# Optimization experiments

Hardware: AMD Instinct MI355X
Metric: run time of the kernel (lower is better)

The kernel has to match this reference:

```python
import jax, jax.numpy as jnp
import numpy as np

N = 50000      # nodes
E = 800000     # edges
F = 128        # node feature dim (= output_size, residual)
H = 128        # hidden_size

def _uniform_fan_avg(key, shape):
    # VarianceScaling(scale=1.0, mode='fan_avg', distribution='uniform')
    fan_avg = (shape[0] + shape[1]) / 2.0
    limit = np.sqrt(3.0 / fan_avg)
    return jax.random.uniform(key, shape, jnp.float32, -limit, limit)

def setup_inputs() -> dict:
    key = jax.random.key(0)
    ks = jax.random.split(key, 16)
    h = jax.random.normal(ks[0], (N, F), jnp.float32)
    pos = jax.random.normal(ks[1], (N, 3), jnp.float32)
    senders = jax.random.randint(ks[2], (E,), 0, N, jnp.int32)
    receivers = jax.random.randint(ks[3], (E,), 0, N, jnp.int32)
    # edge_mlp: Linear(2F+1 -> H) silu, Linear(H -> H) silu (activate_final=True)
    eW1 = _uniform_fan_avg(ks[4], (2 * F + 1, H)); eb1 = jnp.zeros((H,), jnp.float32)
    eW2 = _uniform_fan_avg(ks[5], (H, H)); eb2 = jnp.zeros((H,), jnp.float32)
    # node_mlp: Linear(F+H -> H) silu, Linear(H -> F) (no final act)
    nW1 = _uniform_fan_avg(ks[6], (F + H, H)); nb1 = jnp.zeros((H,), jnp.float32)
    nW2 = _uniform_fan_avg(ks[7], (H, F)); nb2 = jnp.zeros((F,), jnp.float32)
    # pos_correction_mlp: Linear(H -> H) silu, Linear(H -> 1, no bias, UniformScaling(dt))
    pW1 = _uniform_fan_avg(ks[8], (H, H)); pb1 = jnp.zeros((H,), jnp.float32)
    dt = 0.001
    pW2 = jax.random.uniform(ks[9], (H, 1), jnp.float32, -dt, dt) * np.sqrt(3.0)
    return {"h": h, "pos": pos, "senders": senders, "receivers": receivers,
            "eW1": eW1, "eb1": eb1, "eW2": eW2, "eb2": eb2,
            "nW1": nW1, "nb1": nb1, "nW2": nW2, "nb2": nb2,
            "pW1": pW1, "pb1": pb1, "pW2": pW2}

def reference(h, pos, senders, receivers,
              eW1, eb1, eW2, eb2,
              nW1, nb1, nW2, nb2,
              pW1, pb1, pW2):
    n = h.shape[0]
    # _coord2radial (normalize=False)
    coord_diff = pos[senders] - pos[receivers]            # [E,3]
    radial = jnp.sum(coord_diff ** 2, axis=1, keepdims=True)  # [E,1]
    # edge update (_message): concat(h[senders], h[receivers], radial) -> edge_mlp
    msg_in = jnp.concatenate([h[senders], h[receivers], radial], axis=-1)  # [E,2F+1]
    msg = jax.nn.silu(msg_in @ eW1 + eb1)
    msg = jax.nn.silu(msg @ eW2 + eb2)                    # [E,H]
    # node update (_update): aggregate messages at receivers, node_mlp, residual
    agg = jax.ops.segment_sum(msg, receivers, num_segments=n)  # [N,H]
    x = jnp.concatenate([h, agg], axis=-1)                # [N,F+H]
    x = jax.nn.silu(x @ nW1 + nb1)
    x = x @ nW2 + nb2                                     # [N,F]
    h_new = h + x                                         # residual
    # position update (_pos_update)
    pc = jax.nn.silu(msg @ pW1 + pb1) @ pW2               # [E,1]
    trans = jnp.clip(coord_diff * pc, -100, 100)          # [E,3]
    pos_new = pos + jax.ops.segment_sum(trans, senders, num_segments=n)
    return h_new, pos_new
```

## Files before the change

### kernel.cpp

```cpp
#include <hip/hip_runtime.h>
#include <hip/hip_bf16.h>

#define NNODES 50000
#define NEDGES 800000
#define EB 1024
#define SCAN_BLOCKS 196
#define TRN_BLOCKS 448

typedef short bf16x8 __attribute__((ext_vector_type(8)));
typedef float f32x4 __attribute__((ext_vector_type(4)));
typedef unsigned short u16;
typedef unsigned int u32;

__device__ __forceinline__ u16 f2bf(float f) {
    __hip_bfloat16 b = __float2bfloat16(f);
    return *reinterpret_cast<u16*>(&b);
}
__device__ __forceinline__ float bf2f(u16 v) {
    u32 u = ((u32)v) << 16;
    return __uint_as_float(u);
}
__device__ __forceinline__ u32 pack2(float a, float b) {
    __hip_bfloat162 t = __float22bfloat162_rn(float2{a, b});
    return *reinterpret_cast<u32*>(&t);
}
__device__ __forceinline__ float fast_silu(float x) {
    float e = __builtin_amdgcn_exp2f(-1.442695040888963f * x);
    return x * __builtin_amdgcn_rcpf(1.0f + e);
}
__device__ __forceinline__ bf16x8 ld8(const u16* p) {
    return *(const bf16x8*)p;
}
__device__ __forceinline__ f32x4 mfma16(bf16x8 a, bf16x8 b, f32x4 c) {
    return __builtin_amdgcn_mfma_f32_16x16x32_bf16(a, b, c, 0, 0, 0);
}

__global__ void prep_kernel(const float* __restrict__ eW1, const float* __restrict__ eW2,
                            const float* __restrict__ pW1, const float* __restrict__ nW1,
                            const float* __restrict__ nW2,
                            u16* __restrict__ eW1T, u16* __restrict__ eW2T,
                            u16* __restrict__ pW1T, u16* __restrict__ nW1T,
                            u16* __restrict__ nW2T,
                            const int* __restrict__ rcv, int* __restrict__ counts) {
    int b = blockIdx.x;
    if (b < TRN_BLOCKS) {
        int i = b * 256 + threadIdx.x;
        const float* src; u16* dst; int K;
        if (i < 32768)      { src = eW1; dst = eW1T; K = 256; }
        else if (i < 49152) { src = eW2; dst = eW2T; K = 128; i -= 32768; }
        else if (i < 65536) { src = pW1; dst = pW1T; K = 128; i -= 49152; }
        else if (i < 98304) { src = nW1; dst = nW1T; K = 256; i -= 65536; }
        else                { src = nW2; dst = nW2T; K = 128; i -= 98304; }
        int n = i / K, k = i - n * K;
        dst[i] = f2bf(src[k * 128 + n]);
    } else {
        int e = (b - TRN_BLOCKS) * 256 + threadIdx.x;
        if (e < NEDGES) atomicAdd(&counts[rcv[e]], 1);
    }
}

__global__ __launch_bounds__(256) void gemm_p(
    const float* __restrict__ h, const u16* __restrict__ eW1T,
    const u16* __restrict__ nW1T, const float* __restrict__ eb1,
    u16* __restrict__ P)
{
    const int tid  = threadIdx.x;
    const int w    = tid >> 6;
    const int lane = tid & 63;
    const int m    = lane & 15;
    const int quad = lane >> 4;
    const int ksub = quad * 8;

    bf16x8 bw[4][6];
    float bias[6];
    #pragma unroll
    for (int cc = 0; cc < 6; cc++) {
        int C = 96 * w + 16 * cc + m;
        const u16* bp;
        if (C < 128)      { bp = eW1T + C * 256;               bias[cc] = 0.5f * eb1[C]; }
        else if (C < 256) { bp = eW1T + (C - 128) * 256 + 128; bias[cc] = 0.5f * eb1[C - 128]; }
        else              { bp = nW1T + (C - 256) * 256;       bias[cc] = 0.f; }
        #pragma unroll
        for (int t = 0; t < 4; t++) bw[t][cc] = ld8(bp + t * 32 + ksub);
    }
    const int base = blockIdx.x * 64;
    #pragma unroll
    for (int mt = 0; mt < 4; mt++) {
        int nm = base + mt * 16 + m;
        if (nm >= NNODES) nm = NNODES - 1;
        bf16x8 afr[4];
        #pragma unroll
        for (int t = 0; t < 4; t++) {
            const float* ap = h + (size_t)nm * 128 + t * 32 + ksub;
            f32x4 lo = *(const f32x4*)ap;
            f32x4 hi = *(const f32x4*)(ap + 4);
            #pragma unroll
            for (int j = 0; j < 4; j++) {
                afr[t][j]     = (short)f2bf(lo[j]);
                afr[t][4 + j] = (short)f2bf(hi[j]);
            }
        }
        f32x4 acc[6];
        #pragma unroll
        for (int cc = 0; cc < 6; cc++) acc[cc] = (f32x4){0,0,0,0};
        #pragma unroll
        for (int t = 0; t < 4; t++)
            #pragma unroll
            for (int cc = 0; cc < 6; cc++)
                acc[cc] = mfma16(afr[t], bw[t][cc], acc[cc]);
        #pragma unroll
        for (int cc = 0; cc < 6; cc++) {
            int C = 96 * w + 16 * cc + m;
            #pragma unroll
            for (int r = 0; r < 4; r++) {
                int nr = base + mt * 16 + quad * 4 + r;
                if (nr < NNODES) P[(size_t)nr * 384 + C] = f2bf(acc[cc][r] + bias[cc]);
            }
        }
    }
}

__global__ void scan1(const int* __restrict__ counts, int* __restrict__ excl,
                      int* __restrict__ blkSum) {
    __shared__ int tmp[256];
    int tx = threadIdx.x;
    int i = blockIdx.x * 256 + tx;
    int v = (i < NNODES) ? counts[i] : 0;
    tmp[tx] = v;
    __syncthreads();
    for (int off = 1; off < 256; off <<= 1) {
        int t = (tx >= off) ? tmp[tx - off] : 0;
        __syncthreads();
        tmp[tx] += t;
        __syncthreads();
    }
    if (i < NNODES) excl[i] = tmp[tx] - v;
    if (tx == 255) blkSum[blockIdx.x] = tmp[255];
}
__global__ void scan2(const int* __restrict__ blkSum, int* __restrict__ blkOff) {
    __shared__ int tmp[256];
    int tx = threadIdx.x;
    int v = (tx < SCAN_BLOCKS) ? blkSum[tx] : 0;
    tmp[tx] = v;
    __syncthreads();
    for (int off = 1; off < 256; off <<= 1) {
        int t = (tx >= off) ? tmp[tx - off] : 0;
        __syncthreads();
        tmp[tx] += t;
        __syncthreads();
    }
    if (tx < SCAN_BLOCKS) blkOff[tx] = tmp[tx] - v;
}
__global__ void scan3(const int* __restrict__ excl, const int* __restrict__ blkOff,
                      int* __restrict__ cursor) {
    int i = blockIdx.x * 256 + threadIdx.x;
    if (i < NNODES) cursor[i] = excl[i] + blkOff[blockIdx.x];
}
__global__ void scatter_kernel(const int* __restrict__ rcv, int* __restrict__ cursor,
                               int* __restrict__ perm) {
    int e = blockIdx.x * 256 + threadIdx.x;
    if (e < NEDGES) {
        int p = atomicAdd(&cursor[rcv[e]], 1);
        perm[p] = e;
    }
}

struct __align__(16) EdgeLds {
    u16   m1[64 * 136];
    u16   msg[64 * 136];
    float diff[64][4];
    float pcpart[4][64];
    float wlast[128];
    float radial[64];
    int   sndloc[64];
    int   rcvloc[64];
};

__global__ __launch_bounds__(256, 4) void edge_kernel(
    const u16* __restrict__ P, const float* __restrict__ pos,
    const int* __restrict__ snd, const int* __restrict__ rcv,
    const int* __restrict__ perm,
    const float* __restrict__ eW1last,
    const u16* __restrict__ eW2T, const float* __restrict__ eb2,
    const u16* __restrict__ pW1T, const float* __restrict__ pb1,
    const float* __restrict__ pW2,
    float* __restrict__ agg, float* __restrict__ posacc)
{
    __shared__ EdgeLds S;
    const int tid  = threadIdx.x;
    const int w    = tid >> 6;
    const int lane = tid & 63;
    const int m    = lane & 15;
    const int quad = lane >> 4;
    const int ksub = quad * 8;

    bf16x8 bw2[4][2], bp1[4][2];
    float b2v[2], pb1v[2], pw2v[2];
    #pragma unroll
    for (int cc = 0; cc < 2; cc++) {
        int col = (2 * w + cc) * 16 + m;
        #pragma unroll
        for (int t = 0; t < 4; t++) {
            bw2[t][cc] = ld8(eW2T + col * 128 + t * 32 + ksub);
            bp1[t][cc] = ld8(pW1T + col * 128 + t * 32 + ksub);
        }
        b2v[cc]  = eb2[col];
        pb1v[cc] = pb1[col];
        pw2v[cc] = pW2[col];
    }
    if (tid < 128) S.wlast[tid] = eW1last[tid];

    for (int base = blockIdx.x * 64; base < NEDGES; base += gridDim.x * 64) {
        __syncthreads();
        const int e = lane;
        int eg = perm[base + e];
        int s = snd[eg], r = rcv[eg];
        if (tid < 64) {
            S.sndloc[tid] = s; S.rcvloc[tid] = r;
            float rad = 0.f;
            #pragma unroll
            for (int c = 0; c < 3; c++) {
                float d = pos[s * 3 + c] - pos[r * 3 + c];
                S.diff[tid][c] = d;
                rad += d * d;
            }
            S.radial[tid] = rad;
        }
        __syncthreads();
        {
            float rad = S.radial[e];
            const u16* pa = P + (size_t)s * 384 + w * 32;
            const u16* pb = P + (size_t)r * 384 + 128 + w * 32;
            const int sw = e >> 3;
            #pragma unroll
            for (int k = 0; k < 4; k++) {
                bf16x8 va = ld8(pa + k * 8);
                bf16x8 vb = ld8(pb + k * 8);
                u32 pk[4];
                #pragma unroll
                for (int jj = 0; jj < 4; jj++) {
                    int col = w * 32 + k * 8 + jj * 2;
                    float2 wl = *(const float2*)&S.wlast[col];
                    float v0 = bf2f((u16)va[jj * 2])     + bf2f((u16)vb[jj * 2])     + rad * wl.x;
                    float v1 = bf2f((u16)va[jj * 2 + 1]) + bf2f((u16)vb[jj * 2 + 1]) + rad * wl.y;
                    pk[jj] = pack2(fast_silu(v0), fast_silu(v1));
                }
                int chunk = (w * 4 + k) ^ sw;
                *(uint4*)&S.m1[e * 136 + chunk * 8] =
                    make_uint4(pk[0], pk[1], pk[2], pk[3]);
            }
        }
        __syncthreads();
        #pragma unroll
        for (int mt = 0; mt < 4; mt++) {
            const int rs = mt * 2 + (m >> 3);
            const int row = mt * 16 + m;
            f32x4 acc0 = (f32x4){0,0,0,0}, acc1 = (f32x4){0,0,0,0};
            #pragma unroll
            for (int t = 0; t < 4; t++) {
                bf16x8 a = *(const bf16x8*)&S.m1[row * 136 + ((t * 4 + quad) ^ rs) * 8];
                acc0 = mfma16(a, bw2[t][0], acc0);
                acc1 = mfma16(a, bw2[t][1], acc1);
            }
            #pragma unroll
            for (int cc = 0; cc < 2; cc++) {
                f32x4 acc = cc ? acc1 : acc0;
                int col = (2 * w + cc) * 16 + m;
                #pragma unroll
                for (int rr = 0; rr < 4; rr++) {
                    int orow = mt * 16 + quad * 4 + rr;
                    S.msg[orow * 136 + col] = f2bf(fast_silu(acc[rr] + b2v[cc]));
                }
            }
        }
        __syncthreads();
        #pragma unroll
        for (int mt = 0; mt < 4; mt++) {
            f32x4 acc0 = (f32x4){0,0,0,0}, acc1 = (f32x4){0,0,0,0};
            #pragma unroll
            for (int t = 0; t < 4; t++) {
                bf16x8 a = *(const bf16x8*)&S.msg[(mt * 16 + m) * 136 + t * 32 + ksub];
                acc0 = mfma16(a, bp1[t][0], acc0);
                acc1 = mfma16(a, bp1[t][1], acc1);
            }
            float p4[4];
            #pragma unroll
            for (int rr = 0; rr < 4; rr++)
                p4[rr] = fast_silu(acc0[rr] + pb1v[0]) * pw2v[0]
                       + fast_silu(acc1[rr] + pb1v[1]) * pw2v[1];
            #pragma unroll
            for (int mask = 1; mask < 16; mask <<= 1) {
                #pragma unroll
                for (int rr = 0; rr < 4; rr++) p4[rr] += __shfl_xor(p4[rr], mask);
            }
            if (m == 0) {
                #pragma unroll
                for (int rr = 0; rr < 4; rr++)
                    S.pcpart[w][mt * 16 + quad * 4 + rr] = p4[rr];
            }
        }
        {
            int half = tid >> 7, col = tid & 127;
            int r0 = half * 32;
            float a = 0.f;
            int cur = S.rcvloc[r0];
            for (int rr = r0; rr < r0 + 32; ++rr) {
                int rc = S.rcvloc[rr];
                if (rc != cur) {
                    atomicAdd(&agg[(size_t)cur * 128 + col], a);
                    a = 0.f; cur = rc;
                }
                a += bf2f(S.msg[rr * 136 + col]);
            }
            atomicAdd(&agg[(size_t)cur * 128 + col], a);
        }
        __syncthreads();
        if (tid < 192) {
            int ee = tid / 3, c = tid - ee * 3;
            float pc = S.pcpart[0][ee] + S.pcpart[1][ee] + S.pcpart[2][ee] + S.pcpart[3][ee];
            float tr = S.diff[ee][c] * pc;
            tr = fminf(fmaxf(tr, -100.f), 100.f);
            atomicAdd(&posacc[S.sndloc[ee] * 3 + c], tr);
        }
    }
}

__global__ __launch_bounds__(256, 4) void node_kernel(
    const u16* __restrict__ P, const float* __restrict__ h,
    const float* __restrict__ agg,
    const u16* __restrict__ nW1T, const float* __restrict__ nb1,
    const u16* __restrict__ nW2T, const float* __restrict__ nb2,
    const float* __restrict__ pos, const float* __restrict__ posacc,
    float* __restrict__ out)
{
    __shared__ alignas(16) u16 m1[64 * 136];
    const int tid  = threadIdx.x;
    const int w    = tid >> 6;
    const int lane = tid & 63;
    const int m    = lane & 15;
    const int quad = lane >> 4;
    const int ksub = quad * 8;

    bf16x8 bw1[4][2], bw2[4][2];
    float b1v[2], b2v[2];
    #pragma unroll
    for (int cc = 0; cc < 2; cc++) {
        int col = (2 * w + cc) * 16 + m;
        #pragma unroll
        for (int t = 0; t < 4; t++) {
            bw1[t][cc] = ld8(nW1T + col * 256 + 128 + t * 32 + ksub);
            bw2[t][cc] = ld8(nW2T + col * 128 + t * 32 + ksub);
        }
        b1v[cc] = nb1[col];
        b2v[cc] = nb2[col];
    }
    const int base = blockIdx.x * 64;
    #pragma unroll
    for (int mt = 0; mt < 4; mt++) {
        int nm = base + mt * 16 + m;
        if (nm >= NNODES) nm = NNODES - 1;
        f32x4 acc0 = (f32x4){0,0,0,0}, acc1 = (f32x4){0,0,0,0};
        #pragma unroll
        for (int t = 0; t < 4; t++) {
            const float* ap = agg + (size_t)nm * 128 + t * 32 + ksub;
            f32x4 lo = *(const f32x4*)ap;
            f32x4 hi = *(const f32x4*)(ap + 4);
            bf16x8 a;
            #pragma unroll
            for (int j = 0; j < 4; j++) {
                a[j]     = (short)f2bf(lo[j]);
                a[4 + j] = (short)f2bf(hi[j]);
            }
            acc0 = mfma16(a, bw1[t][0], acc0);
            acc1 = mfma16(a, bw1[t][1], acc1);
        }
        #pragma unroll
        for (int cc = 0; cc < 2; cc++) {
            f32x4 acc = cc ? acc1 : acc0;
            int col = (2 * w + cc) * 16 + m;
            #pragma unroll
            for (int rr = 0; rr < 4; rr++) {
                int row = mt * 16 + quad * 4 + rr;
                int nrc = base + row; if (nrc >= NNODES) nrc = NNODES - 1;
                float v = acc[rr] + bf2f(P[(size_t)nrc * 384 + 256 + col]) + b1v[cc];
                m1[row * 136 + col] = f2bf(fast_silu(v));
            }
        }
    }
    __syncthreads();
    #pragma unroll
    for (int mt = 0; mt < 4; mt++) {
        f32x4 acc0 = (f32x4){0,0,0,0}, acc1 = (f32x4){0,0,0,0};
        #pragma unroll
        for (int t = 0; t < 4; t++) {
            bf16x8 a = *(const bf16x8*)&m1[(mt * 16 + m) * 136 + t * 32 + ksub];
            acc0 = mfma16(a, bw2[t][0], acc0);
            acc1 = mfma16(a, bw2[t][1], acc1);
        }
        #pragma unroll
        for (int cc = 0; cc < 2; cc++) {
            f32x4 acc = cc ? acc1 : acc0;
            int col = (2 * w + cc) * 16 + m;
            #pragma unroll
            for (int rr = 0; rr < 4; rr++) {
                int nr = base + mt * 16 + quad * 4 + rr;
                if (nr < NNODES)
                    out[(size_t)nr * 128 + col] = acc[rr] + b2v[cc] + h[(size_t)nr * 128 + col];
            }
        }
    }
    if (tid < 192) {
        int i = blockIdx.x * 192 + tid;
        if (i < NNODES * 3) out[NNODES * 128 + i] = pos[i] + posacc[i];
    }
}

extern "C" void kernel_launch(void* const* d_in, const int* in_sizes, int n_in,
                              void* d_out, int out_size, void* d_ws, size_t ws_size,
                              hipStream_t stream) {
    (void)in_sizes; (void)n_in; (void)out_size; (void)ws_size;
    const float* h   = (const float*)d_in[0];
    const float* pos = (const float*)d_in[1];
    const int*   snd = (const int*)d_in[2];
    const int*   rcv = (const int*)d_in[3];
    const float* eW1 = (const float*)d_in[4];
    const float* eb1 = (const float*)d_in[5];
    const float* eW2 = (const float*)d_in[6];
    const float* eb2 = (const float*)d_in[7];
    const float* nW1 = (const float*)d_in[8];
    const float* nb1 = (const float*)d_in[9];
    const float* nW2 = (const float*)d_in[10];
    const float* nb2 = (const float*)d_in[11];
    const float* pW1 = (const float*)d_in[12];
    const float* pb1 = (const float*)d_in[13];
    const float* pW2 = (const float*)d_in[14];
    float* out = (float*)d_out;

    float* agg    = (float*)d_ws;
    float* posacc = agg + (size_t)NNODES * 128;
    u16* P    = (u16*)(posacc + (size_t)NNODES * 3);
    u16* eW1T = P + (size_t)NNODES * 384;
    u16* eW2T = eW1T + 128 * 256;
    u16* pW1T = eW2T + 128 * 128;
    u16* nW1T = pW1T + 128 * 128;
    u16* nW2T = nW1T + 128 * 256;
    int* counts = (int*)(nW2T + 128 * 128);
    int* excl   = counts + 50048;
    int* blkSum = excl + 50048;
    int* blkOff = blkSum + 256;
    int* cursor = blkOff + 256;
    int* perm   = cursor + 50048;

    hipMemsetAsync(agg, 0, (size_t)NNODES * 131 * sizeof(float), stream);
    hipMemsetAsync(counts, 0, 50048 * sizeof(int), stream);

    prep_kernel<<<TRN_BLOCKS + (NEDGES + 255) / 256, 256, 0, stream>>>(
        eW1, eW2, pW1, nW1, nW2, eW1T, eW2T, pW1T, nW1T, nW2T, rcv, counts);

    gemm_p<<<(NNODES + 63) / 64, 256, 0, stream>>>(h, eW1T, nW1T, eb1, P);

    scan1<<<SCAN_BLOCKS, 256, 0, stream>>>(counts, excl, blkSum);
    scan2<<<1, 256, 0, stream>>>(blkSum, blkOff);
    scan3<<<SCAN_BLOCKS, 256, 0, stream>>>(excl, blkOff, cursor);
    scatter_kernel<<<(NEDGES + 255) / 256, 256, 0, stream>>>(rcv, cursor, perm);

    edge_kernel<<<EB, 256, 0, stream>>>(
        P, pos, snd, rcv, perm,
        eW1 + 256 * 128,
        eW2T, eb2, pW1T, pb1, pW2,
        agg, posacc);

    node_kernel<<<(NNODES + 63) / 64, 256, 0, stream>>>(
        P, h, agg, nW1T, nb1, nW2T, nb2, pos, posacc, out);
}
```

Measured before the change: 449.8 us.

## Fuse all stages into one cooperative persistent kernel with grid-wide phases

Replaces the chain of separate launches and memsets (weight transpose, count, gemm, three scan kernels, scatter, edge, node) with a single persistent kernel that runs each stage as a phase, separated by grid syncs when cooperative launch is available. It also zeroes the accumulators in-kernel, overlaps edge counting with the node GEMM, and merges scan3 into the scatter by adding block offsets inline. The goal is to remove per-launch overhead and idle gaps between small kernels. In exchange, grid syncs add cost, the grid is limited to what fits resident (which may lower occupancy), and the GEMM phase reloads weights per tile in halves.

```diff
diff --git a/kernel.cpp b/kernel.cpp
--- a/kernel.cpp
+++ b/kernel.cpp
@@ -1,11 +1,14 @@
 #include <hip/hip_runtime.h>
 #include <hip/hip_bf16.h>
+#include <hip/hip_cooperative_groups.h>
+
+namespace cg = cooperative_groups;
 
 #define NNODES 50000
 #define NEDGES 800000
-#define EB 1024
-#define SCAN_BLOCKS 196
-#define TRN_BLOCKS 448
+#define NTILE_N 782
+#define TRN_ITEMS 114688
+#define ZWORDS4 1650012
 
 typedef short bf16x8 __attribute__((ext_vector_type(8)));
 typedef float f32x4 __attribute__((ext_vector_type(4)));
@@ -35,135 +38,15 @@
     return __builtin_amdgcn_mfma_f32_16x16x32_bf16(a, b, c, 0, 0, 0);
 }
 
-__global__ void prep_kernel(const float* __restrict__ eW1, const float* __restrict__ eW2,
-                            const float* __restrict__ pW1, const float* __restrict__ nW1,
-                            const float* __restrict__ nW2,
-                            u16* __restrict__ eW1T, u16* __restrict__ eW2T,
-                            u16* __restrict__ pW1T, u16* __restrict__ nW1T,
-                            u16* __restrict__ nW2T,
-                            const int* __restrict__ rcv, int* __restrict__ counts) {
-    int b = blockIdx.x;
-    if (b < TRN_BLOCKS) {
-        int i = b * 256 + threadIdx.x;
-        const float* src; u16* dst; int K;
-        if (i < 32768)      { src = eW1; dst = eW1T; K = 256; }
-        else if (i < 49152) { src = eW2; dst = eW2T; K = 128; i -= 32768; }
-        else if (i < 65536) { src = pW1; dst = pW1T; K = 128; i -= 49152; }
-        else if (i < 98304) { src = nW1; dst = nW1T; K = 256; i -= 65536; }
-        else                { src = nW2; dst = nW2T; K = 128; i -= 98304; }
-        int n = i / K, k = i - n * K;
-        dst[i] = f2bf(src[k * 128 + n]);
-    } else {
-        int e = (b - TRN_BLOCKS) * 256 + threadIdx.x;
-        if (e < NEDGES) atomicAdd(&counts[rcv[e]], 1);
-    }
-}
-
-__global__ __launch_bounds__(256) void gemm_p(
-    const float* __restrict__ h, const u16* __restrict__ eW1T,
-    const u16* __restrict__ nW1T, const float* __restrict__ eb1,
-    u16* __restrict__ P)
-{
-    const int tid  = threadIdx.x;
-    const int w    = tid >> 6;
-    const int lane = tid & 63;
-    const int m    = lane & 15;
-    const int quad = lane >> 4;
-    const int ksub = quad * 8;
-
-    bf16x8 bw[4][6];
-    float bias[6];
-    #pragma unroll
-    for (int cc = 0; cc < 6; cc++) {
-        int C = 96 * w + 16 * cc + m;
-        const u16* bp;
-        if (C < 128)      { bp = eW1T + C * 256;               bias[cc] = 0.5f * eb1[C]; }
-        else if (C < 256) { bp = eW1T + (C - 128) * 256 + 128; bias[cc] = 0.5f * eb1[C - 128]; }
-        else              { bp = nW1T + (C - 256) * 256;       bias[cc] = 0.f; }
-        #pragma unroll
-        for (int t = 0; t < 4; t++) bw[t][cc] = ld8(bp + t * 32 + ksub);
-    }
-    const int base = blockIdx.x * 64;
-    #pragma unroll
-    for (int mt = 0; mt < 4; mt++) {
-        int nm = base + mt * 16 + m;
-        if (nm >= NNODES) nm = NNODES - 1;
-        bf16x8 afr[4];
-        #pragma unroll
-        for (int t = 0; t < 4; t++) {
-            const float* ap = h + (size_t)nm * 128 + t * 32 + ksub;
-            f32x4 lo = *(const f32x4*)ap;
-            f32x4 hi = *(const f32x4*)(ap + 4);
-            #pragma unroll
-            for (int j = 0; j < 4; j++) {
-                afr[t][j]     = (short)f2bf(lo[j]);
-                afr[t][4 + j] = (short)f2bf(hi[j]);
-            }
-        }
-        f32x4 acc[6];
-        #pragma unroll
-        for (int cc = 0; cc < 6; cc++) acc[cc] = (f32x4){0,0,0,0};
-        #pragma unroll
-        for (int t = 0; t < 4; t++)
-            #pragma unroll
-            for (int cc = 0; cc < 6; cc++)
-                acc[cc] = mfma16(afr[t], bw[t][cc], acc[cc]);
-        #pragma unroll
-        for (int cc = 0; cc < 6; cc++) {
-            int C = 96 * w + 16 * cc + m;
-            #pragma unroll
-            for (int r = 0; r < 4; r++) {
-                int nr = base + mt * 16 + quad * 4 + r;
-                if (nr < NNODES) P[(size_t)nr * 384 + C] = f2bf(acc[cc][r] + bias[cc]);
-            }
-        }
-    }
-}
-
-__global__ void scan1(const int* __restrict__ counts, int* __restrict__ excl,
-                      int* __restrict__ blkSum) {
-    __shared__ int tmp[256];
-    int tx = threadIdx.x;
-    int i = blockIdx.x * 256 + tx;
-    int v = (i < NNODES) ? counts[i] : 0;
-    tmp[tx] = v;
-    __syncthreads();
-    for (int off = 1; off < 256; off <<= 1) {
-        int t = (tx >= off) ? tmp[tx - off] : 0;
-        __syncthreads();
-        tmp[tx] += t;
-        __syncthreads();
-    }
-    if (i < NNODES) excl[i] = tmp[tx] - v;
-    if (tx == 255) blkSum[blockIdx.x] = tmp[255];
-}
-__global__ void scan2(const int* __restrict__ blkSum, int* __restrict__ blkOff) {
-    __shared__ int tmp[256];
-    int tx = threadIdx.x;
-    int v = (tx < SCAN_BLOCKS) ? blkSum[tx] : 0;
-    tmp[tx] = v;
-    __syncthreads();
-    for (int off = 1; off < 256; off <<= 1) {
-        int t = (tx >= off) ? tmp[tx - off] : 0;
-        __syncthreads();
-        tmp[tx] += t;
-        __syncthreads();
-    }
-    if (tx < SCAN_BLOCKS) blkOff[tx] = tmp[tx] - v;
-}
-__global__ void scan3(const int* __restrict__ excl, const int* __restrict__ blkOff,
-                      int* __restrict__ cursor) {
-    int i = blockIdx.x * 256 + threadIdx.x;
-    if (i < NNODES) cursor[i] = excl[i] + blkOff[blockIdx.x];
-}
-__global__ void scatter_kernel(const int* __restrict__ rcv, int* __restrict__ cursor,
-                               int* __restrict__ perm) {
-    int e = blockIdx.x * 256 + threadIdx.x;
-    if (e < NEDGES) {
-        int p = atomicAdd(&cursor[rcv[e]], 1);
-        perm[p] = e;
-    }
-}
+struct MegaParams {
+    const float *h, *pos;
+    const int *snd, *rcv;
+    const float *eW1, *eb1, *eW2, *eb2, *nW1, *nb1, *nW2, *nb2, *pW1, *pb1, *pW2;
+    float *agg, *posacc;
+    int *counts, *excl, *blkSum, *blkOff, *perm;
+    u16 *P, *eW1T, *eW2T, *pW1T, *nW1T, *nW2T;
+    float *out;
+};
 
 struct __align__(16) EdgeLds {
     u16   m1[64 * 136];
@@ -176,242 +59,338 @@
     int   rcvloc[64];
 };
 
-__global__ __launch_bounds__(256, 4) void edge_kernel(
-    const u16* __restrict__ P, const float* __restrict__ pos,
-    const int* __restrict__ snd, const int* __restrict__ rcv,
-    const int* __restrict__ perm,
-    const float* __restrict__ eW1last,
-    const u16* __restrict__ eW2T, const float* __restrict__ eb2,
-    const u16* __restrict__ pW1T, const float* __restrict__ pb1,
-    const float* __restrict__ pW2,
-    float* __restrict__ agg, float* __restrict__ posacc)
-{
-    __shared__ EdgeLds S;
+union SharedU {
+    EdgeLds edge;
+    int     scan[256];
+    u16     nm1[64 * 136];
+};
+
+__global__ __launch_bounds__(256, 4) void mega(MegaParams p, int plo, int phi) {
+    __shared__ SharedU U;
     const int tid  = threadIdx.x;
+    const int gid  = blockIdx.x * 256 + tid;
+    const int gsz  = gridDim.x * 256;
     const int w    = tid >> 6;
     const int lane = tid & 63;
     const int m    = lane & 15;
     const int quad = lane >> 4;
     const int ksub = quad * 8;
 
-    bf16x8 bw2[4][2], bp1[4][2];
-    float b2v[2], pb1v[2], pw2v[2];
-    #pragma unroll
-    for (int cc = 0; cc < 2; cc++) {
-        int col = (2 * w + cc) * 16 + m;
-        #pragma unroll
-        for (int t = 0; t < 4; t++) {
-            bw2[t][cc] = ld8(eW2T + col * 128 + t * 32 + ksub);
-            bp1[t][cc] = ld8(pW1T + col * 128 + t * 32 + ksub);
-        }
-        b2v[cc]  = eb2[col];
-        pb1v[cc] = pb1[col];
-        pw2v[cc] = pW2[col];
-    }
-    if (tid < 128) S.wlast[tid] = eW1last[tid];
-
-    for (int base = blockIdx.x * 64; base < NEDGES; base += gridDim.x * 64) {
-        __syncthreads();
-        const int e = lane;
-        int eg = perm[base + e];
-        int s = snd[eg], r = rcv[eg];
-        if (tid < 64) {
-            S.sndloc[tid] = s; S.rcvloc[tid] = r;
-            float rad = 0.f;
-            #pragma unroll
-            for (int c = 0; c < 3; c++) {
-                float d = pos[s * 3 + c] - pos[r * 3 + c];
-                S.diff[tid][c] = d;
-                rad += d * d;
-            }
-            S.radial[tid] = rad;
-        }
-        __syncthreads();
-        {
-            float rad = S.radial[e];
-            const u16* pa = P + (size_t)s * 384 + w * 32;
-            const u16* pb = P + (size_t)r * 384 + 128 + w * 32;
-            const int sw = e >> 3;
-            #pragma unroll
-            for (int k = 0; k < 4; k++) {
-                bf16x8 va = ld8(pa + k * 8);
-                bf16x8 vb = ld8(pb + k * 8);
-                u32 pk[4];
-                #pragma unroll
-                for (int jj = 0; jj < 4; jj++) {
-                    int col = w * 32 + k * 8 + jj * 2;
-                    float2 wl = *(const float2*)&S.wlast[col];
-                    float v0 = bf2f((u16)va[jj * 2])     + bf2f((u16)vb[jj * 2])     + rad * wl.x;
-                    float v1 = bf2f((u16)va[jj * 2 + 1]) + bf2f((u16)vb[jj * 2 + 1]) + rad * wl.y;
-                    pk[jj] = pack2(fast_silu(v0), fast_silu(v1));
-                }
-                int chunk = (w * 4 + k) ^ sw;
-                *(uint4*)&S.m1[e * 136 + chunk * 8] =
-                    make_uint4(pk[0], pk[1], pk[2], pk[3]);
-            }
-        }
-        __syncthreads();
-        #pragma unroll
-        for (int mt = 0; mt < 4; mt++) {
-            const int rs = mt * 2 + (m >> 3);
-            const int row = mt * 16 + m;
-            f32x4 acc0 = (f32x4){0,0,0,0}, acc1 = (f32x4){0,0,0,0};
-            #pragma unroll
-            for (int t = 0; t < 4; t++) {
-                bf16x8 a = *(const bf16x8*)&S.m1[row * 136 + ((t * 4 + quad) ^ rs) * 8];
-                acc0 = mfma16(a, bw2[t][0], acc0);
-                acc1 = mfma16(a, bw2[t][1], acc1);
-            }
+    for (int ph = plo; ph <= phi; ph++) {
+        if (ph == 1) {
+            f32x4* z = (f32x4*)p.agg;
+            for (int i = gid; i < ZWORDS4; i += gsz) z[i] = (f32x4){0,0,0,0};
+            for (int i = gid; i < TRN_ITEMS; i += gsz) {
+                int j = i, n, k;
+                const float* src; u16* dst;
+                if (i < 32768)       { src = p.eW1; dst = p.eW1T; n = j >> 8; k = j & 255; }
+                else if (i < 49152)  { j -= 32768; src = p.eW2; dst = p.eW2T; n = j >> 7; k = j & 127; }
+                else if (i < 65536)  { j -= 49152; src = p.pW1; dst = p.pW1T; n = j >> 7; k = j & 127; }
+                else if (i < 98304)  { j -= 65536; src = p.nW1; dst = p.nW1T; n = j >> 8; k = j & 255; }
+                else                 { j -= 98304; src = p.nW2; dst = p.nW2T; n = j >> 7; k = j & 127; }
+                dst[j] = f2bf(src[k * 128 + n]);
+            }
+        } else if (ph == 2) {
+            for (int e = gid; e < NEDGES; e += gsz)
+                atomicAdd(&p.counts[p.rcv[e]], 1);
+            for (int it = blockIdx.x; it < NTILE_N; it += gridDim.x) {
+                const int base = it * 64;
+                #pragma unroll
+                for (int half = 0; half < 2; half++) {
+                    bf16x8 bw[4][3];
+                    float bias[3];
+                    #pragma unroll
+                    for (int cc = 0; cc < 3; cc++) {
+                        int C = 96 * w + 48 * half + 16 * cc + m;
+                        const u16* bp;
+                        if (C < 128)      { bp = p.eW1T + C * 256;               bias[cc] = 0.5f * p.eb1[C]; }
+                        else if (C < 256) { bp = p.eW1T + (C - 128) * 256 + 128; bias[cc] = 0.5f * p.eb1[C - 128]; }
+                        else              { bp = p.nW1T + (C - 256) * 256;       bias[cc] = 0.f; }
+                        #pragma unroll
+                        for (int t = 0; t < 4; t++) bw[t][cc] = ld8(bp + t * 32 + ksub);
+                    }
+                    #pragma unroll
+                    for (int mt = 0; mt < 4; mt++) {
+                        int nm = base + mt * 16 + m;
+                        if (nm >= NNODES) nm = NNODES - 1;
+                        bf16x8 afr[4];
+                        #pragma unroll
+                        for (int t = 0; t < 4; t++) {
+                            const float* ap = p.h + (size_t)nm * 128 + t * 32 + ksub;
+                            f32x4 lo = *(const f32x4*)ap;
+                            f32x4 hi = *(const f32x4*)(ap + 4);
+                            #pragma unroll
+                            for (int j = 0; j < 4; j++) {
+                                afr[t][j]     = (short)f2bf(lo[j]);
+                                afr[t][4 + j] = (short)f2bf(hi[j]);
+                            }
+                        }
+                        f32x4 acc[3];
+                        #pragma unroll
+                        for (int cc = 0; cc < 3; cc++) acc[cc] = (f32x4){0,0,0,0};
+                        #pragma unroll
+                        for (int t = 0; t < 4; t++)
+                            #pragma unroll
+                            for (int cc = 0; cc < 3; cc++)
+                                acc[cc] = mfma16(afr[t], bw[t][cc], acc[cc]);
+                        #pragma unroll
+                        for (int cc = 0; cc < 3; cc++) {
+                            int C = 96 * w + 48 * half + 16 * cc + m;
+                            #pragma unroll
+                            for (int r = 0; r < 4; r++) {
+                                int nr = base + mt * 16 + quad * 4 + r;
+                                if (nr < NNODES) p.P[(size_t)nr * 384 + C] = f2bf(acc[cc][r] + bias[cc]);
+                            }
+                        }
+                    }
+                }
+            }
+        } else if (ph == 3) {
+            for (int b = blockIdx.x; b < 196; b += gridDim.x) {
+                __syncthreads();
+                int i = b * 256 + tid;
+                int v = (i < NNODES) ? p.counts[i] : 0;
+                U.scan[tid] = v;
+                __syncthreads();
+                for (int off = 1; off < 256; off <<= 1) {
+                    int t = (tid >= off) ? U.scan[tid - off] : 0;
+                    __syncthreads();
+                    U.scan[tid] += t;
+                    __syncthreads();
+                }
+                if (i < NNODES) p.excl[i] = U.scan[tid] - v;
+                if (tid == 255) p.blkSum[b] = U.scan[255];
+            }
+        } else if (ph == 4) {
+            if (blockIdx.x == 0) {
+                int v = (tid < 196) ? p.blkSum[tid] : 0;
+                U.scan[tid] = v;
+                __syncthreads();
+                for (int off = 1; off < 256; off <<= 1) {
+                    int t = (tid >= off) ? U.scan[tid - off] : 0;
+                    __syncthreads();
+                    U.scan[tid] += t;
+                    __syncthreads();
+                }
+                if (tid < 196) p.blkOff[tid] = U.scan[tid] - v;
+            }
+        } else if (ph == 5) {
+            for (int e = gid; e < NEDGES; e += gsz) {
+                int r = p.rcv[e];
+                int pi = atomicAdd(&p.excl[r], 1) + p.blkOff[r >> 8];
+                p.perm[pi] = e;
+            }
+        } else if (ph == 6) {
+            EdgeLds& S = U.edge;
+            const float* eW1last = p.eW1 + 256 * 128;
+            bf16x8 bw2[4][2], bp1[4][2];
+            float b2v[2], pb1v[2], pw2v[2];
             #pragma unroll
             for (int cc = 0; cc < 2; cc++) {
-                f32x4 acc = cc ? acc1 : acc0;
                 int col = (2 * w + cc) * 16 + m;
                 #pragma unroll
-                for (int rr = 0; rr < 4; rr++) {
-                    int orow = mt * 16 + quad * 4 + rr;
-                    S.msg[orow * 136 + col] = f2bf(fast_silu(acc[rr] + b2v[cc]));
-                }
-            }
+                for (int t = 0; t < 4; t++) {
+                    bw2[t][cc] = ld8(p.eW2T + col * 128 + t * 32 + ksub);
+                    bp1[t][cc] = ld8(p.pW1T + col * 128 + t * 32 + ksub);
+                }
+                b2v[cc]  = p.eb2[col];
+                pb1v[cc] = p.pb1[col];
+                pw2v[cc] = p.pW2[col];
+            }
+            if (tid < 128) S.wlast[tid] = eW1last[tid];
+
+            for (int base = blockIdx.x * 64; base < NEDGES; base += gridDim.x * 64) {
+                __syncthreads();
+                const int e = lane;
+                int eg = p.perm[base + e];
+                int s = p.snd[eg], r = p.rcv[eg];
+                if (tid < 64) {
+                    S.sndloc[tid] = s; S.rcvloc[tid] = r;
+                    float rad = 0.f;
+                    #pragma unroll
+                    for (int c = 0; c < 3; c++) {
+                        float d = p.pos[s * 3 + c] - p.pos[r * 3 + c];
+                        S.diff[tid][c] = d;
+                        rad += d * d;
+                    }
+                    S.radial[tid] = rad;
+                }
+                __syncthreads();
+                {
+                    float rad = S.radial[e];
+                    const u16* pa = p.P + (size_t)s * 384 + w * 32;
+                    const u16* pb = p.P + (size_t)r * 384 + 128 + w * 32;
+                    const int sw = e >> 3;
+                    #pragma unroll
+                    for (int k = 0; k < 4; k++) {
+                        bf16x8 va = ld8(pa + k * 8);
+                        bf16x8 vb = ld8(pb + k * 8);
+                        u32 pk[4];
+                        #pragma unroll
+                        for (int jj = 0; jj < 4; jj++) {
+                            int col = w * 32 + k * 8 + jj * 2;
+                            float2 wl = *(const float2*)&S.wlast[col];
+                            float v0 = bf2f((u16)va[jj * 2])     + bf2f((u16)vb[jj * 2])     + rad * wl.x;
+                            float v1 = bf2f((u16)va[jj * 2 + 1]) + bf2f((u16)vb[jj * 2 + 1]) + rad * wl.y;
+                            pk[jj] = pack2(fast_silu(v0), fast_silu(v1));
+                        }
+                        int chunk = (w * 4 + k) ^ sw;
+                        *(uint4*)&S.m1[e * 136 + chunk * 8] =
+                            make_uint4(pk[0], pk[1], pk[2], pk[3]);
+                    }
+                }
+                __syncthreads();
+                #pragma unroll
+                for (int mt = 0; mt < 4; mt++) {
+                    const int rs = mt * 2 + (m >> 3);
+                    const int row = mt * 16 + m;
+                    f32x4 acc0 = (f32x4){0,0,0,0}, acc1 = (f32x4){0,0,0,0};
+                    #pragma unroll
+                    for (int t = 0; t < 4; t++) {
+                        bf16x8 a = *(const bf16x8*)&S.m1[row * 136 + ((t * 4 + quad) ^ rs) * 8];
+                        acc0 = mfma16(a, bw2[t][0], acc0);
+                        acc1 = mfma16(a, bw2[t][1], acc1);
+                    }
+                    #pragma unroll
+                    for (int cc = 0; cc < 2; cc++) {
+                        f32x4 acc = cc ? acc1 : acc0;
+                        int col = (2 * w + cc) * 16 + m;
+                        #pragma unroll
+                        for (int rr = 0; rr < 4; rr++) {
+                            int orow = mt * 16 + quad * 4 + rr;
+                            S.msg[orow * 136 + col] = f2bf(fast_silu(acc[rr] + b2v[cc]));
+                        }
+                    }
+                }
+                __syncthreads();
+                #pragma unroll
+                for (int mt = 0; mt < 4; mt++) {
+                    f32x4 acc0 = (f32x4){0,0,0,0}, acc1 = (f32x4){0,0,0,0};
+                    #pragma unroll
+                    for (int t = 0; t < 4; t++) {
+                        bf16x8 a = *(const bf16x8*)&S.msg[(mt * 16 + m) * 136 + t * 32 + ksub];
+                        acc0 = mfma16(a, bp1[t][0], acc0);
+                        acc1 = mfma16(a, bp1[t][1], acc1);
+                    }
+                    float p4[4];
+                    #pragma unroll
+                    for (int rr = 0; rr < 4; rr++)
+                        p4[rr] = fast_silu(acc0[rr] + pb1v[0]) * pw2v[0]
+                               + fast_silu(acc1[rr] + pb1v[1]) * pw2v[1];
+                    #pragma unroll
+                    for (int mask = 1; mask < 16; mask <<= 1) {
+                        #pragma unroll
+                        for (int rr = 0; rr < 4; rr++) p4[rr] += __shfl_xor(p4[rr], mask);
+                    }
+                    if (m == 0) {
+                        #pragma unroll
+                        for (int rr = 0; rr < 4; rr++)
+                            S.pcpart[w][mt * 16 + quad * 4 + rr] = p4[rr];
+                    }
+                }
+                {
+                    int half = tid >> 7, col = tid & 127;
+                    int r0 = half * 32;
+                    float a = 0.f;
+                    int cur = S.rcvloc[r0];
+                    for (int rr = r0; rr < r0 + 32; ++rr) {
+                        int rc = S.rcvloc[rr];
+                        if (rc != cur) {
+                            atomicAdd(&p.agg[(size_t)cur * 128 + col], a);
+                            a = 0.f; cur = rc;
+                        }
+                        a += bf2f(S.msg[rr * 136 + col]);
+                    }
+                    atomicAdd(&p.agg[(size_t)cur * 128 + col], a);
+                }
+                __syncthreads();
+                if (tid < 192) {
+                    int ee = tid / 3, c = tid - ee * 3;
+                    float pc = S.pcpart[0][ee] + S.pcpart[1][ee] + S.pcpart[2][ee] + S.pcpart[3][ee];
+                    float tr = S.diff[ee][c] * pc;
+                    tr = fminf(fmaxf(tr, -100.f), 100.f);
+                    atomicAdd(&p.posacc[S.sndloc[ee] * 3 + c], tr);
+                }
+            }
+        } else if (ph == 7) {
+            bf16x8 bw1[4][2], bw2[4][2];
+            float b1v[2], b2v[2];
+            #pragma unroll
+            for (int cc = 0; cc < 2; cc++) {
+                int col = (2 * w + cc) * 16 + m;
+                #pragma unroll
+                for (int t = 0; t < 4; t++) {
+                    bw1[t][cc] = ld8(p.nW1T + col * 256 + 128 + t * 32 + ksub);
+                    bw2[t][cc] = ld8(p.nW2T + col * 128 + t * 32 + ksub);
+                }
+                b1v[cc] = p.nb1[col];
+                b2v[cc] = p.nb2[col];
+            }
+            for (int it = blockIdx.x; it < NTILE_N; it += gridDim.x) {
+                const int base = it * 64;
+                __syncthreads();
+                #pragma unroll
+                for (int mt = 0; mt < 4; mt++) {
+                    int nm = base + mt * 16 + m;
+                    if (nm >= NNODES) nm = NNODES - 1;
+                    f32x4 acc0 = (f32x4){0,0,0,0}, acc1 = (f32x4){0,0,0,0};
+                    #pragma unroll
+                    for (int t = 0; t < 4; t++) {
+                        const float* ap = p.agg + (size_t)nm * 128 + t * 32 + ksub;
+                        f32x4 lo = *(const f32x4*)ap;
+                        f32x4 hi = *(const f32x4*)(ap + 4);
+                        bf16x8 a;
+                        #pragma unroll
+                        for (int j = 0; j < 4; j++) {
+                            a[j]     = (short)f2bf(lo[j]);
+                            a[4 + j] = (short)f2bf(hi[j]);
+                        }
+                        acc0 = mfma16(a, bw1[t][0], acc0);
+                        acc1 = mfma16(a, bw1[t][1], acc1);
+                    }
+                    #pragma unroll
+                    for (int cc = 0; cc < 2; cc++) {
+                        f32x4 acc = cc ? acc1 : acc0;
+                        int col = (2 * w + cc) * 16 + m;
+                        #pragma unroll
+                        for (int rr = 0; rr < 4; rr++) {
+                            int row = mt * 16 + quad * 4 + rr;
+                            int nrc = base + row; if (nrc >= NNODES) nrc = NNODES - 1;
+                            float v = acc[rr] + bf2f(p.P[(size_t)nrc * 384 + 256 + col]) + b1v[cc];
+                            U.nm1[row * 136 + col] = f2bf(fast_silu(v));
+                        }
+                    }
+                }
+                __syncthreads();
+                #pragma unroll
+                for (int mt = 0; mt < 4; mt++) {
+                    f32x4 acc0 = (f32x4){0,0,0,0}, acc1 = (f32x4){0,0,0,0};
+                    #pragma unroll
+                    for (int t = 0; t < 4; t++) {
+                        bf16x8 a = *(const bf16x8*)&U.nm1[(mt * 16 + m) * 136 + t * 32 + ksub];
+                        acc0 = mfma16(a, bw2[t][0], acc0);
+                        acc1 = mfma16(a, bw2[t][1], acc1);
+                    }
+                    #pragma unroll
+                    for (int cc = 0; cc < 2; cc++) {
+                        f32x4 acc = cc ? acc1 : acc0;
+                        int col = (2 * w + cc) * 16 + m;
+                        #pragma unroll
+                        for (int rr = 0; rr < 4; rr++) {
+                            int nr = base + mt * 16 + quad * 4 + rr;
+                            if (nr < NNODES)
+                                p.out[(size_t)nr * 128 + col] = acc[rr] + b2v[cc] + p.h[(size_t)nr * 128 + col];
+                        }
+                    }
+                }
+            }
+            for (int i = gid; i < NNODES * 3; i += gsz)
+                p.out[(size_t)NNODES * 128 + i] = p.pos[i] + p.posacc[i];
         }
-        __syncthreads();
-        #pragma unroll
-        for (int mt = 0; mt < 4; mt++) {
-            f32x4 acc0 = (f32x4){0,0,0,0}, acc1 = (f32x4){0,0,0,0};
-            #pragma unroll
-            for (int t = 0; t < 4; t++) {
-                bf16x8 a = *(const bf16x8*)&S.msg[(mt * 16 + m) * 136 + t * 32 + ksub];
-                acc0 = mfma16(a, bp1[t][0], acc0);
-                acc1 = mfma16(a, bp1[t][1], acc1);
-            }
-            float p4[4];
-            #pragma unroll
-            for (int rr = 0; rr < 4; rr++)
-                p4[rr] = fast_silu(acc0[rr] + pb1v[0]) * pw2v[0]
-                       + fast_silu(acc1[rr] + pb1v[1]) * pw2v[1];
-            #pragma unroll
-            for (int mask = 1; mask < 16; mask <<= 1) {
-                #pragma unroll
-                for (int rr = 0; rr < 4; rr++) p4[rr] += __shfl_xor(p4[rr], mask);
-            }
-            if (m == 0) {
-                #pragma unroll
-                for (int rr = 0; rr < 4; rr++)
-                    S.pcpart[w][mt * 16 + quad * 4 + rr] = p4[rr];
-            }
+        if (ph != phi) {
+            __threadfence();
+            cg::this_grid().sync();
         }
-        {
-            int half = tid >> 7, col = tid & 127;
-            int r0 = half * 32;
-            float a = 0.f;
-            int cur = S.rcvloc[r0];
-            for (int rr = r0; rr < r0 + 32; ++rr) {
-                int rc = S.rcvloc[rr];
-                if (rc != cur) {
-                    atomicAdd(&agg[(size_t)cur * 128 + col], a);
-                    a = 0.f; cur = rc;
-                }
-                a += bf2f(S.msg[rr * 136 + col]);
-            }
-            atomicAdd(&agg[(size_t)cur * 128 + col], a);
-        }
-        __syncthreads();
-        if (tid < 192) {
-            int ee = tid / 3, c = tid - ee * 3;
-            float pc = S.pcpart[0][ee] + S.pcpart[1][ee] + S.pcpart[2][ee] + S.pcpart[3][ee];
-            float tr = S.diff[ee][c] * pc;
-            tr = fminf(fmaxf(tr, -100.f), 100.f);
-            atomicAdd(&posacc[S.sndloc[ee] * 3 + c], tr);
-        }
-    }
-}
-
-__global__ __launch_bounds__(256, 4) void node_kernel(
-    const u16* __restrict__ P, const float* __restrict__ h,
-    const float* __restrict__ agg,
-    const u16* __restrict__ nW1T, const float* __restrict__ nb1,
-    const u16* __restrict__ nW2T, const float* __restrict__ nb2,
-    const float* __restrict__ pos, const float* __restrict__ posacc,
-    float* __restrict__ out)
-{
-    __shared__ alignas(16) u16 m1[64 * 136];
-    const int tid  = threadIdx.x;
-    const int w    = tid >> 6;
-    const int lane = tid & 63;
-    const int m    = lane & 15;
-    const int quad = lane >> 4;
-    const int ksub = quad * 8;
-
-    bf16x8 bw1[4][2], bw2[4][2];
-    float b1v[2], b2v[2];
-    #pragma unroll
-    for (int cc = 0; cc < 2; cc++) {
-        int col = (2 * w + cc) * 16 + m;
-        #pragma unroll
-        for (int t = 0; t < 4; t++) {
-            bw1[t][cc] = ld8(nW1T + col * 256 + 128 + t * 32 + ksub);
-            bw2[t][cc] = ld8(nW2T + col * 128 + t * 32 + ksub);
-        }
-        b1v[cc] = nb1[col];
-        b2v[cc] = nb2[col];
-    }
-    const int base = blockIdx.x * 64;
-    #pragma unroll
-    for (int mt = 0; mt < 4; mt++) {
-        int nm = base + mt * 16 + m;
-        if (nm >= NNODES) nm = NNODES - 1;
-        f32x4 acc0 = (f32x4){0,0,0,0}, acc1 = (f32x4){0,0,0,0};
-        #pragma unroll
-        for (int t = 0; t < 4; t++) {
-            const float* ap = agg + (size_t)nm * 128 + t * 32 + ksub;
-            f32x4 lo = *(const f32x4*)ap;
-            f32x4 hi = *(const f32x4*)(ap + 4);
-            bf16x8 a;
-            #pragma unroll
-            for (int j = 0; j < 4; j++) {
-                a[j]     = (short)f2bf(lo[j]);
-                a[4 + j] = (short)f2bf(hi[j]);
-            }
-            acc0 = mfma16(a, bw1[t][0], acc0);
-            acc1 = mfma16(a, bw1[t][1], acc1);
-        }
-        #pragma unroll
-        for (int cc = 0; cc < 2; cc++) {
-            f32x4 acc = cc ? acc1 : acc0;
-            int col = (2 * w + cc) * 16 + m;
-            #pragma unroll
-            for (int rr = 0; rr < 4; rr++) {
-                int row = mt * 16 + quad * 4 + rr;
-                int nrc = base + row; if (nrc >= NNODES) nrc = NNODES - 1;
-                float v = acc[rr] + bf2f(P[(size_t)nrc * 384 + 256 + col]) + b1v[cc];
-                m1[row * 136 + col] = f2bf(fast_silu(v));
-            }
-        }
-    }
-    __syncthreads();
-    #pragma unroll
-    for (int mt = 0; mt < 4; mt++) {
-        f32x4 acc0 = (f32x4){0,0,0,0}, acc1 = (f32x4){0,0,0,0};
-        #pragma unroll
-        for (int t = 0; t < 4; t++) {
-            bf16x8 a = *(const bf16x8*)&m1[(mt * 16 + m) * 136 + t * 32 + ksub];
-            acc0 = mfma16(a, bw2[t][0], acc0);
-            acc1 = mfma16(a, bw2[t][1], acc1);
-        }
-        #pragma unroll
-        for (int cc = 0; cc < 2; cc++) {
-            f32x4 acc = cc ? acc1 : acc0;
-            int col = (2 * w + cc) * 16 + m;
-            #pragma unroll
-            for (int rr = 0; rr < 4; rr++) {
-                int nr = base + mt * 16 + quad * 4 + rr;
-                if (nr < NNODES)
-                    out[(size_t)nr * 128 + col] = acc[rr] + b2v[cc] + h[(size_t)nr * 128 + col];
-            }
-        }
-    }
-    if (tid < 192) {
-        int i = blockIdx.x * 192 + tid;
-        if (i < NNODES * 3) out[NNODES * 128 + i] = pos[i] + posacc[i];
     }
 }
 
@@ -419,57 +398,62 @@
                               void* d_out, int out_size, void* d_ws, size_t ws_size,
                               hipStream_t stream) {
     (void)in_sizes; (void)n_in; (void)out_size; (void)ws_size;
-    const float* h   = (const float*)d_in[0];
-    const float* pos = (const float*)d_in[1];
-    const int*   snd = (const int*)d_in[2];
-    const int*   rcv = (const int*)d_in[3];
-    const float* eW1 = (const float*)d_in[4];
-    const float* eb1 = (const float*)d_in[5];
-    const float* eW2 = (const float*)d_in[6];
-    const float* eb2 = (const float*)d_in[7];
-    const float* nW1 = (const float*)d_in[8];
-    const float* nb1 = (const float*)d_in[9];
-    const float* nW2 = (const float*)d_in[10];
-    const float* nb2 = (const float*)d_in[11];
-    const float* pW1 = (const float*)d_in[12];
-    const float* pb1 = (const float*)d_in[13];
-    const float* pW2 = (const float*)d_in[14];
-    float* out = (float*)d_out;
-
-    float* agg    = (float*)d_ws;
-    float* posacc = agg + (size_t)NNODES * 128;
-    u16* P    = (u16*)(posacc + (size_t)NNODES * 3);
-    u16* eW1T = P + (size_t)NNODES * 384;
-    u16* eW2T = eW1T + 128 * 256;
-    u16* pW1T = eW2T + 128 * 128;
-    u16* nW1T = pW1T + 128 * 128;
-    u16* nW2T = nW1T + 128 * 256;
-    int* counts = (int*)(nW2T + 128 * 128);
-    int* excl   = counts + 50048;
-    int* blkSum = excl + 50048;
-    int* blkOff = blkSum + 256;
-    int* cursor = blkOff + 256;
-    int* perm   = cursor + 50048;
-
-    hipMemsetAsync(agg, 0, (size_t)NNODES * 131 * sizeof(float), stream);
-    hipMemsetAsync(counts, 0, 50048 * sizeof(int), stream);
-
-    prep_kernel<<<TRN_BLOCKS + (NEDGES + 255) / 256, 256, 0, stream>>>(
-        eW1, eW2, pW1, nW1, nW2, eW1T, eW2T, pW1T, nW1T, nW2T, rcv, counts);
-
-    gemm_p<<<(NNODES + 63) / 64, 256, 0, stream>>>(h, eW1T, nW1T, eb1, P);
-
-    scan1<<<SCAN_BLOCKS, 256, 0, stream>>>(counts, excl, blkSum);
-    scan2<<<1, 256, 0, stream>>>(blkSum, blkOff);
-    scan3<<<SCAN_BLOCKS, 256, 0, stream>>>(excl, blkOff, cursor);
-    scatter_kernel<<<(NEDGES + 255) / 256, 256, 0, stream>>>(rcv, cursor, perm);
-
-    edge_kernel<<<EB, 256, 0, stream>>>(
-        P, pos, snd, rcv, perm,
-        eW1 + 256 * 128,
-        eW2T, eb2, pW1T, pb1, pW2,
-        agg, posacc);
-
-    node_kernel<<<(NNODES + 63) / 64, 256, 0, stream>>>(
-        P, h, agg, nW1T, nb1, nW2T, nb2, pos, posacc, out);
-}
+    MegaParams p;
+    p.h   = (const float*)d_in[0];
+    p.pos = (const float*)d_in[1];
+    p.snd = (const int*)d_in[2];
+    p.rcv = (const int*)d_in[3];
+    p.eW1 = (const float*)d_in[4];
+    p.eb1 = (const float*)d_in[5];
+    p.eW2 = (const float*)d_in[6];
+    p.eb2 = (const float*)d_in[7];
+    p.nW1 = (const float*)d_in[8];
+    p.nb1 = (const float*)d_in[9];
+    p.nW2 = (const float*)d_in[10];
+    p.nb2 = (const float*)d_in[11];
+    p.pW1 = (const float*)d_in[12];
+    p.pb1 = (const float*)d_in[13];
+    p.pW2 = (const float*)d_in[14];
+    p.out = (float*)d_out;
+
+    p.agg    = (float*)d_ws;
+    p.posacc = p.agg + (size_t)NNODES * 128;
+    p.counts = (int*)(p.posacc + (size_t)NNODES * 3);
+    p.excl   = p.counts + 50048;
+    p.blkSum = p.excl + 50048;
+    p.blkOff = p.blkSum + 256;
+    p.perm   = p.blkOff + 256;
+    p.P      = (u16*)(p.perm + NEDGES);
+    p.eW1T   = p.P + (size_t)NNODES * 384;
+    p.eW2T   = p.eW1T + 128 * 256;
+    p.pW1T   = p.eW2T + 128 * 128;
+    p.nW1T   = p.pW1T + 128 * 128;
+    p.nW2T   = p.nW1T + 128 * 256;
+
+    int dev = 0;
+    hipGetDevice(&dev);
+    int coop = 0, ncu = 0;
+    hipDeviceGetAttribute(&coop, hipDeviceAttributeCooperativeLaunch, dev);
+    hipDeviceGetAttribute(&ncu, hipDeviceAttributeMultiprocessorCount, dev);
+
+    bool done = false;
+    if (coop && ncu > 0) {
+        int maxB = 0;
+        hipError_t oe = hipOccupancyMaxActiveBlocksPerMultiprocessor(
+            &maxB, (const void*)mega, 256, 0);
+        if (oe == hipSuccess && maxB > 0) {
+            int grid = maxB * ncu;
+            if (grid > 1024) grid = 1024;
+            int plo = 1, phi = 7;
+            void* args[] = {(void*)&p, (void*)&plo, (void*)&phi};
+            hipError_t le = hipLaunchCooperativeKernel((const void*)mega, dim3(grid),
+                                                       dim3(256), args, 0, stream);
+            done = (le == hipSuccess);
+        }
+    }
+    if (!done) {
+        static const int grids[8] = {0, 2048, 3904, 196, 1, 3125, 1024, 1024};
+        for (int ph = 1; ph <= 7; ph++)
+            mega<<<grids[ph], 256, 0, stream>>>(p, ph, ph);
+    }
+}
```

Result: slower. 1.460 ms (+224.5%).
